# Performance work log

Measured on AMD Instinct MI355X. Metric: run time of the kernel, lower is better.

The kernel has to match this reference:

```python
import jax, jax.numpy as jnp
import numpy as np

DIM = 1024
NUM_HEADS = 16
HEAD_DIM = 64

def setup_inputs() -> dict:
    key = jax.random.key(0)
    ks = jax.random.split(key, 7)
    x = jax.random.normal(ks[0], (4, 4096, DIM), dtype=jnp.float32)
    mask = jnp.ones((4, 4096), dtype=jnp.float32)
    # torch Linear stores weight (out, in) and computes x @ W.T; we store (in, out) directly.
    Wq = jax.random.normal(ks[1], (DIM, NUM_HEADS * HEAD_DIM), dtype=jnp.float32) / np.sqrt(DIM)
    Wk = jax.random.normal(ks[2], (DIM, NUM_HEADS * HEAD_DIM), dtype=jnp.float32) / np.sqrt(DIM)
    Wv = jax.random.normal(ks[3], (DIM, NUM_HEADS * HEAD_DIM), dtype=jnp.float32) / np.sqrt(DIM)
    Wo = jax.random.normal(ks[4], (NUM_HEADS * HEAD_DIM, DIM), dtype=jnp.float32) / np.sqrt(NUM_HEADS * HEAD_DIM)
    # FeatureMap buffer: randn(dim, dim) / sqrt(dim) with dim = head_dim
    proj = jax.random.normal(ks[5], (HEAD_DIM, HEAD_DIM), dtype=jnp.float32) / np.sqrt(HEAD_DIM)
    return {"x": x, "mask": mask, "Wq": Wq, "Wk": Wk, "Wv": Wv, "Wo": Wo, "proj": proj}

def _feature_map(x, proj):
    # phi(x) = elu(x @ proj) + 1  (non-negative random features)
    return jax.nn.elu(x @ proj) + 1.0

def reference(x, mask, Wq, Wk, Wv, Wo, proj):
    b, n, _ = x.shape
    h, d = NUM_HEADS, HEAD_DIM
    # project and split heads: (b, h, n, d)
    q = (x @ Wq).reshape(b, n, h, d).transpose(0, 2, 1, 3)
    k = (x @ Wk).reshape(b, n, h, d).transpose(0, 2, 1, 3)
    v = (x @ Wv).reshape(b, n, h, d).transpose(0, 2, 1, 3)
    q = _feature_map(q, proj)
    k = _feature_map(k, proj)
    # mask: (b, n) -> (b, 1, n, 1)
    k = k * mask[:, None, :, None]
    # linear attention: phi(Q) (phi(K)^T V)
    kv = jnp.einsum('bhnd,bhne->bhde', k, v)          # (b, h, d, d)
    qkv = jnp.einsum('bhnd,bhde->bhne', q, kv)        # (b, h, n, d)
    k_sum = k.sum(axis=2)                              # (b, h, d)
    normalizer = jnp.einsum('bhnd,bhd->bhn', q, k_sum) + 1e-06
    out = qkv / normalizer[..., None]
    out = out.transpose(0, 2, 1, 3).reshape(b, n, h * d)
    return out @ Wo
```

## Files before the change

### kernel.cpp

```cpp
#include <hip/hip_runtime.h>
#include <stdint.h>

#define TOKENS 16384
#define KDIM 1024
#define QKVN 3072

typedef unsigned short u16;
using bf16x8 = __attribute__((ext_vector_type(8))) __bf16;
using f32x4  = __attribute__((ext_vector_type(4))) float;
using u16x8  = __attribute__((ext_vector_type(8))) unsigned short;

__device__ inline u16 f2bf(float f) {
  union { float f; uint32_t u; } v; v.f = f;
  uint32_t u = v.u;
  return (u16)((u + 0x7FFFu + ((u >> 16) & 1u)) >> 16);
}
__device__ inline float bf2f(u16 s) {
  union { uint32_t u; float f; } v; v.u = ((uint32_t)s) << 16;
  return v.f;
}
__device__ inline void g2l16(const void* g, void* l) {
  __builtin_amdgcn_global_load_lds(
      (const __attribute__((address_space(1))) void*)g,
      (__attribute__((address_space(3))) void*)l, 16, 0, 0);
}

template<int LD>
__device__ inline void stage_half(const u16* __restrict__ g, u16* l, int t) {
  #pragma unroll
  for (int i = 0; i < 2; ++i) {
    const int ch = i * 512 + t;
    const int row = ch >> 3;
    const int cc = (ch & 7) ^ (row & 7);
    g2l16(g + (long)row * LD + cc * 8, (char*)l + ch * 16);
  }
}

#define LDA_H(DST, BASE) do { \
  _Pragma("unroll") \
  for (int mi = 0; mi < 4; ++mi) { \
    const int row = wm*64 + mi*16 + rl; \
    const char* p = (const char*)(BASE) + row*128; \
    const int sw = (row & 7) << 4; \
    DST[mi][0] = *(const bf16x8*)(p + ((kg*16) ^ sw)); \
    DST[mi][1] = *(const bf16x8*)(p + ((64 + kg*16) ^ sw)); \
  } \
} while (0)

#define LDB_H(DST, BASE) do { \
  _Pragma("unroll") \
  for (int ni = 0; ni < 2; ++ni) { \
    const int row = wn*32 + ni*16 + rl; \
    const char* p = (const char*)(BASE) + row*128; \
    const int sw = (row & 7) << 4; \
    DST[ni][0] = *(const bf16x8*)(p + ((kg*16) ^ sw)); \
    DST[ni][1] = *(const bf16x8*)(p + ((64 + kg*16) ^ sw)); \
  } \
} while (0)

#define MFMAQ(MH, NH, AV, BV) do { \
  __builtin_amdgcn_s_setprio(1); \
  _Pragma("unroll") \
  for (int kh = 0; kh < 2; ++kh) \
    _Pragma("unroll") \
    for (int mi = 0; mi < 4; ++mi) \
      _Pragma("unroll") \
      for (int ni = 0; ni < 2; ++ni) \
        acc[(MH)*4+mi][(NH)*2+ni] = __builtin_amdgcn_mfma_f32_16x16x32_bf16( \
            AV[mi][kh], BV[ni][kh], acc[(MH)*4+mi][(NH)*2+ni], 0, 0, 0); \
  __builtin_amdgcn_s_setprio(0); \
} while (0)

#define LGKM0 do { \
  asm volatile("s_waitcnt lgkmcnt(0)" ::: "memory"); \
  __builtin_amdgcn_sched_barrier(0); \
} while (0)
#define LGKM_PRE(N) asm volatile("s_waitcnt lgkmcnt(" #N ")" ::: "memory")
#define VMC(N) asm volatile("s_waitcnt vmcnt(" #N ")" ::: "memory")
#define BAR() __builtin_amdgcn_s_barrier()

template<int NTOT, int EPI, int ALD, int NT, int PERB>
__global__ __launch_bounds__(512, 2) void gemm256(
    const u16* __restrict__ A, const u16* __restrict__ Bm,
    void* __restrict__ C, const float* __restrict__ aux) {
  __shared__ u16 As[2][2][8192];
  __shared__ u16 Bs[2][2][8192];
  const int t = threadIdx.x;
  const int l = t & 63;
  const int w = t >> 6;
  const int rl = l & 15, kg = l >> 4;
  const int wm = w >> 2, wn = w & 3;
  constexpr int nbn = NTOT / 256;
  constexpr int nwg = 64 * nbn;
  constexpr int GRID = nwg / NT;
  constexpr int KC = NT * 16;
  constexpr int IT = KC / 2;
  static_assert(nwg % 8 == 0, "bijective xcd swizzle");
  const int bid = blockIdx.x;

  auto tcoord = [&](int ot, long& tar, long& tbr) {
    const int gt = ot * GRID + bid;
    const int swz = (gt & 7) * (nwg / 8) + (gt >> 3);
    tar = (long)(swz / nbn) * 256;
    tbr = (long)(swz % nbn) * 256;
  };
  auto asrc = [&](int ch) {
    long ta, tb; tcoord(ch >> 4, ta, tb);
    return A + ta * ALD + (ch & 15) * 64;
  };
  auto bsrc = [&](int ch) {
    long ta, tb; tcoord(ch >> 4, ta, tb);
    return Bm + (PERB ? (ta >> 12) * 1048576 : 0) + tb * 1024 + (ch & 15) * 64;
  };

  f32x4 acc[8][4];
  #pragma unroll
  for (int i = 0; i < 8; ++i)
    #pragma unroll
    for (int j = 0; j < 4; ++j)
      acc[i][j] = (f32x4){0.f, 0.f, 0.f, 0.f};

  bf16x8 af[4][2], b0[2][2], b1[2][2];

  auto epilogue = [&](int ot) {
    long ar0, br0; tcoord(ot, ar0, br0);
    #pragma unroll
    for (int mh = 0; mh < 2; ++mh)
      #pragma unroll
      for (int mi = 0; mi < 4; ++mi)
        #pragma unroll
        for (int j = 0; j < 4; ++j) {
          const long row = ar0 + mh*128 + wm*64 + mi*16 + kg*4 + j;
          float rs = 0.f;
          if (EPI == 0) rs = aux[row];
          #pragma unroll
          for (int nh = 0; nh < 2; ++nh)
            #pragma unroll
            for (int ni = 0; ni < 2; ++ni) {
              const long col = br0 + nh*128 + wn*32 + ni*16 + rl;
              float v = acc[mh*4+mi][nh*2+ni][j];
              if (EPI == 0) {
                if (col < 2048) {
                  v = (v > 0.f) ? (v + 1.f) : __expf(v);
                  if (col >= 1024) v *= rs;
                }
                ((u16*)C)[row * QKVN + col] = f2bf(v);
              } else {
                ((float*)C)[row * NTOT + col] = v;
              }
            }
        }
    #pragma unroll
    for (int i = 0; i < 8; ++i)
      #pragma unroll
      for (int j = 0; j < 4; ++j)
        acc[i][j] = (f32x4){0.f, 0.f, 0.f, 0.f};
  };

  {
    const u16* A0s = asrc(0); const u16* B0s = bsrc(0);
    const u16* A1s = asrc(1); const u16* B1s = bsrc(1);
    stage_half<ALD >(A0s,             As[0][0], t);
    stage_half<1024>(B0s,             Bs[0][0], t);
    stage_half<1024>(B0s + 128*1024,  Bs[0][1], t);
    stage_half<ALD >(A0s + 128*ALD,   As[0][1], t);
    stage_half<ALD >(A1s,             As[1][0], t);
    stage_half<1024>(B1s,             Bs[1][0], t);
    stage_half<1024>(B1s + 128*1024,  Bs[1][1], t);
    VMC(6);
    BAR();
  }

  for (int i = 0; i < IT; ++i) {
    const int e = (2*i + 2 < KC) ? 2*i + 2 : KC - 1;
    const int o = (2*i + 3 < KC) ? 2*i + 3 : KC - 1;
    const u16* Ao1 = asrc(2*i + 1);
    const u16* Ae = asrc(e); const u16* Be = bsrc(e);
    const u16* Ao = asrc(o); const u16* Bo = bsrc(o);

    LDA_H(af, As[0][0]); LDB_H(b0, Bs[0][0]);
    stage_half<ALD>(Ao1 + 128*ALD, As[1][1], t);
    LGKM_PRE(8);
    BAR(); LGKM0;
    MFMAQ(0, 0, af, b0);
    BAR();
    LDB_H(b1, Bs[0][1]);
    stage_half<ALD>(Ae, As[0][0], t);
    BAR(); LGKM0;
    MFMAQ(0, 1, af, b1);
    BAR();
    LDA_H(af, As[0][1]);
    stage_half<1024>(Be, Bs[0][0], t);
    BAR(); LGKM0;
    MFMAQ(1, 0, af, b0);
    BAR();
    stage_half<1024>(Be + 128*1024, Bs[0][1], t);
    BAR();
    MFMAQ(1, 1, af, b1);
    VMC(6);
    BAR();
    LDA_H(af, As[1][0]); LDB_H(b0, Bs[1][0]);
    stage_half<ALD>(Ae + 128*ALD, As[0][1], t);
    LGKM_PRE(8);
    BAR(); LGKM0;
    MFMAQ(0, 0, af, b0);
    BAR();
    LDB_H(b1, Bs[1][1]);
    stage_half<ALD>(Ao, As[1][0], t);
    BAR(); LGKM0;
    MFMAQ(0, 1, af, b1);
    BAR();
    LDA_H(af, As[1][1]);
    stage_half<1024>(Bo, Bs[1][0], t);
    BAR(); LGKM0;
    MFMAQ(1, 0, af, b0);
    BAR();
    stage_half<1024>(Bo + 128*1024, Bs[1][1], t);
    BAR();
    MFMAQ(1, 1, af, b1);
    VMC(6);
    BAR();

    if ((i & 7) == 7) epilogue(i >> 3);
  }
  VMC(0);
}

__global__ __launch_bounds__(256) void kv_kernel(const u16* __restrict__ QKV,
    float* __restrict__ kvws, float* __restrict__ ksws) {
  __shared__ u16 Kl[32 * 64];
  __shared__ u16 Vl[32 * 64];
  const int t = threadIdx.x;
  const int l = t & 63, w = t >> 6;
  const int rl = l & 15, kg = l >> 4;
  const int bid = blockIdx.x;
  const int bh = bid >> 3, ns = bid & 7;
  const int b = bh >> 4, h = bh & 15;
  const long tok0 = (long)b * 4096 + ns * 512;

  f32x4 acc[4];
  #pragma unroll
  for (int i = 0; i < 4; ++i) acc[i] = (f32x4){0.f, 0.f, 0.f, 0.f};
  float ks = 0.f;
  const int srow = t >> 3, scc = t & 7;

  for (int it = 0; it < 16; ++it) {
    const long tb = tok0 + it * 32;
    g2l16(QKV + (tb + srow) * QKVN + 1024 + h * 64 + scc * 8, (char*)Kl + t * 16);
    g2l16(QKV + (tb + srow) * QKVN + 2048 + h * 64 + scc * 8, (char*)Vl + t * 16);
    __syncthreads();
    union { u16x8 u; bf16x8 v; } au, bu;
    #pragma unroll
    for (int j = 0; j < 8; ++j) au.u[j] = Kl[(kg * 8 + j) * 64 + w * 16 + rl];
    #pragma unroll
    for (int ni = 0; ni < 4; ++ni) {
      #pragma unroll
      for (int j = 0; j < 8; ++j) bu.u[j] = Vl[(kg * 8 + j) * 64 + ni * 16 + rl];
      acc[ni] = __builtin_amdgcn_mfma_f32_16x16x32_bf16(au.v, bu.v, acc[ni], 0, 0, 0);
    }
    #pragma unroll
    for (int r = 0; r < 8; ++r) ks += bf2f(Kl[(w * 8 + r) * 64 + (t & 63)]);
    __syncthreads();
  }
  float* kvb = kvws + bh * 4096;
  #pragma unroll
  for (int ni = 0; ni < 4; ++ni)
    #pragma unroll
    for (int j = 0; j < 4; ++j) {
      const int d = w * 16 + kg * 4 + j;
      const int e = ni * 16 + rl;
      atomicAdd(&kvb[d * 64 + e], acc[ni][j]);
    }
  atomicAdd(&ksws[bh * 64 + (t & 63)], ks);
}

__global__ __launch_bounds__(256) void scale_q(u16* __restrict__ QKV,
    const float* __restrict__ ksws) {
  __shared__ float ksl[1024];
  const int bid = blockIdx.x, t = threadIdx.x;
  const int n0 = bid * 16;
  const int b = n0 >> 12;
  #pragma unroll
  for (int i = 0; i < 4; ++i) ksl[i * 256 + t] = ksws[b * 1024 + i * 256 + t];
  __syncthreads();
  const int h = t & 15, ti = t >> 4;
  u16* qp = QKV + (long)(n0 + ti) * QKVN + h * 64;
  u16x8 v[8];
  float norm = 1e-6f;
  #pragma unroll
  for (int i = 0; i < 8; ++i) {
    v[i] = *(const u16x8*)(qp + i * 8);
    #pragma unroll
    for (int j = 0; j < 8; ++j) norm += bf2f(v[i][j]) * ksl[h * 64 + i * 8 + j];
  }
  const float inv = 1.0f / norm;
  #pragma unroll
  for (int i = 0; i < 8; ++i) {
    u16x8 o;
    #pragma unroll
    for (int j = 0; j < 8; ++j) o[j] = f2bf(bf2f(v[i][j]) * inv);
    *(u16x8*)(qp + i * 8) = o;
  }
}

__global__ __launch_bounds__(256) void w2_kernel(const float* __restrict__ kvws,
    const u16* __restrict__ WoT, u16* __restrict__ W2T) {
  __shared__ float kvl[64][64];
  const int bid = blockIdx.x, t = threadIdx.x;
  const int bh = bid >> 2, os = bid & 3;
  const int b = bh >> 4, h = bh & 15;
  const float* kvb = kvws + bh * 4096;
  #pragma unroll
  for (int i = 0; i < 16; ++i) ((float*)kvl)[i * 256 + t] = kvb[i * 256 + t];
  __syncthreads();
  const int o = os * 256 + t;
  float wo[64];
  const u16* wr = WoT + (long)o * 1024 + h * 64;
  #pragma unroll
  for (int i = 0; i < 8; ++i) {
    u16x8 v = *(const u16x8*)(wr + i * 8);
    #pragma unroll
    for (int j = 0; j < 8; ++j) wo[i * 8 + j] = bf2f(v[j]);
  }
  u16* out = W2T + (long)b * 1048576 + (long)o * 1024 + h * 64;
  for (int d = 0; d < 64; ++d) {
    float s = 0.f;
    #pragma unroll
    for (int e = 0; e < 64; ++e) s += wo[e] * kvl[d][e];
    out[d] = f2bf(s);
  }
}

__global__ __launch_bounds__(256) void prep_qk(const float* __restrict__ Wq,
    const float* __restrict__ Wk, const float* __restrict__ proj,
    u16* __restrict__ WqkvT) {
  __shared__ float Wl[128][65];
  __shared__ float Pl[64][65];
  const int bid = blockIdx.x;
  const int m = bid >> 7, h = (bid >> 3) & 15, cb = bid & 7;
  const float* W = m ? Wk : Wq;
  const int t = threadIdx.x;
  #pragma unroll
  for (int i = 0; i < 16; ++i) {
    const int idx = i * 256 + t;
    Pl[idx >> 6][idx & 63] = proj[idx];
  }
  #pragma unroll
  for (int i = 0; i < 32; ++i) {
    const int idx = i * 256 + t;
    const int c = idx >> 6, d = idx & 63;
    Wl[c][d] = W[(long)(cb * 128 + c) * 1024 + h * 64 + d];
  }
  __syncthreads();
  const int c = t & 127, j0 = (t >> 7) * 32;
  float a[32];
  #pragma unroll
  for (int jj = 0; jj < 32; ++jj) a[jj] = 0.f;
  for (int d = 0; d < 64; ++d) {
    const float wv = Wl[c][d];
    #pragma unroll
    for (int jj = 0; jj < 32; ++jj) a[jj] += wv * Pl[d][j0 + jj];
  }
  #pragma unroll
  for (int jj = 0; jj < 32; ++jj)
    WqkvT[(long)(m * 1024 + h * 64 + j0 + jj) * 1024 + cb * 128 + c] = f2bf(a[jj]);
}

__global__ __launch_bounds__(256) void prep_vo(const float* __restrict__ Wv,
    const float* __restrict__ Wo, u16* __restrict__ WqkvT, u16* __restrict__ WoT) {
  __shared__ float til[64][65];
  const int bid = blockIdx.x;
  const int which = bid >> 8, rt = (bid >> 4) & 15, ct = bid & 15;
  const float* S = which ? Wo : Wv;
  const int t = threadIdx.x;
  const int j = t & 63;
  #pragma unroll
  for (int p = 0; p < 16; ++p) {
    const int i = p * 4 + (t >> 6);
    til[i][j] = S[(long)(rt * 64 + i) * 1024 + ct * 64 + j];
  }
  __syncthreads();
  u16* dst = which ? WoT : (WqkvT + (long)2048 * 1024);
  #pragma unroll
  for (int p = 0; p < 16; ++p) {
    const int i = p * 4 + (t >> 6);
    dst[(long)(ct * 64 + i) * 1024 + rt * 64 + j] = f2bf(til[j][i]);
  }
}

__global__ __launch_bounds__(256) void conv_x(const float* __restrict__ x,
                                              u16* __restrict__ xb) {
  const int idx = blockIdx.x * 256 + threadIdx.x;
  const float4* p = (const float4*)x + (long)idx * 2;
  const float4 a = p[0], b = p[1];
  u16x8 o;
  o[0] = f2bf(a.x); o[1] = f2bf(a.y); o[2] = f2bf(a.z); o[3] = f2bf(a.w);
  o[4] = f2bf(b.x); o[5] = f2bf(b.y); o[6] = f2bf(b.z); o[7] = f2bf(b.w);
  *((u16x8*)xb + idx) = o;
}

extern "C" void kernel_launch(void* const* d_in, const int* in_sizes, int n_in,
                              void* d_out, int out_size, void* d_ws, size_t ws_size,
                              hipStream_t stream) {
  const float* x    = (const float*)d_in[0];
  const float* mask = (const float*)d_in[1];
  const float* Wq   = (const float*)d_in[2];
  const float* Wk   = (const float*)d_in[3];
  const float* Wv   = (const float*)d_in[4];
  const float* Wo   = (const float*)d_in[5];
  const float* proj = (const float*)d_in[6];

  char* ws = (char*)d_ws;
  u16*  WqkvT = (u16*)(ws);
  u16*  WoT   = (u16*)(ws + 6291456);
  u16*  xb    = (u16*)(ws + 8388608);
  u16*  QKV   = (u16*)(ws + 41943040);
  float* kvws = (float*)(ws + 142606336);
  float* ksws = (float*)(ws + 143654912);
  u16*  W2T  = (u16*)(ws + 8388608);
  if (ws_size < (size_t)143671296) return;

  hipMemsetAsync(kvws, 0, 1064960, stream);
  prep_qk<<<256, 256, 0, stream>>>(Wq, Wk, proj, WqkvT);
  prep_vo<<<512, 256, 0, stream>>>(Wv, Wo, WqkvT, WoT);
  conv_x <<<8192, 256, 0, stream>>>(x, xb);
  gemm256<3072, 0, 1024, 3, 0><<<256, 512, 0, stream>>>(xb, WqkvT, (void*)QKV, mask);
  kv_kernel<<<512, 256, 0, stream>>>(QKV, kvws, ksws);
  scale_q<<<1024, 256, 0, stream>>>((u16*)QKV, ksws);
  w2_kernel<<<256, 256, 0, stream>>>(kvws, WoT, W2T);
  gemm256<1024, 1, 3072, 1, 1><<<256, 512, 0, stream>>>(QKV, W2T, d_out, nullptr);
}
```

Measured before the change: 277.1 us.

## Restructure GEMM pipeline to four phases; compact Q and drop WoT prep

The GEMM main loop now loads both B halves at once and issues MFMAs across the full N width per phase. This halves the number of barrier-separated phases per k-chunk, at the cost of more live B fragment registers. scale_q writes the normalized Q into a compact 1024-wide buffer so the output GEMM reads A with stride 1024 instead of 3072. The separate Wo transpose/convert pass is removed, and w2_kernel reads fp32 Wo directly with strided loads.

```diff
diff --git a/kernel.cpp b/kernel.cpp
--- a/kernel.cpp
+++ b/kernel.cpp
@@ -58,16 +58,19 @@
   } \
 } while (0)
 
-#define MFMAQ(MH, NH, AV, BV) do { \
+#define MFMA2Q(MH, AV, BV0, BV1) do { \
   __builtin_amdgcn_s_setprio(1); \
   _Pragma("unroll") \
   for (int kh = 0; kh < 2; ++kh) \
     _Pragma("unroll") \
     for (int mi = 0; mi < 4; ++mi) \
       _Pragma("unroll") \
-      for (int ni = 0; ni < 2; ++ni) \
-        acc[(MH)*4+mi][(NH)*2+ni] = __builtin_amdgcn_mfma_f32_16x16x32_bf16( \
-            AV[mi][kh], BV[ni][kh], acc[(MH)*4+mi][(NH)*2+ni], 0, 0, 0); \
+      for (int ni = 0; ni < 2; ++ni) { \
+        acc[(MH)*4+mi][ni]   = __builtin_amdgcn_mfma_f32_16x16x32_bf16( \
+            AV[mi][kh], BV0[ni][kh], acc[(MH)*4+mi][ni], 0, 0, 0); \
+        acc[(MH)*4+mi][2+ni] = __builtin_amdgcn_mfma_f32_16x16x32_bf16( \
+            AV[mi][kh], BV1[ni][kh], acc[(MH)*4+mi][2+ni], 0, 0, 0); \
+      } \
   __builtin_amdgcn_s_setprio(0); \
 } while (0)
 
@@ -120,7 +123,7 @@
     for (int j = 0; j < 4; ++j)
       acc[i][j] = (f32x4){0.f, 0.f, 0.f, 0.f};
 
-  bf16x8 af[4][2], b0[2][2], b1[2][2];
+  bf16x8 afA[4][2], bA[2][2], bB[2][2];
 
   auto epilogue = [&](int ot) {
     long ar0, br0; tcoord(ot, ar0, br0);
@@ -166,60 +169,47 @@
     stage_half<ALD >(A0s + 128*ALD,   As[0][1], t);
     stage_half<ALD >(A1s,             As[1][0], t);
     stage_half<1024>(B1s,             Bs[1][0], t);
-    stage_half<1024>(B1s + 128*1024,  Bs[1][1], t);
-    VMC(6);
+    VMC(4);
     BAR();
   }
 
   for (int i = 0; i < IT; ++i) {
+    const int o1 = 2*i + 1;
     const int e = (2*i + 2 < KC) ? 2*i + 2 : KC - 1;
     const int o = (2*i + 3 < KC) ? 2*i + 3 : KC - 1;
-    const u16* Ao1 = asrc(2*i + 1);
-    const u16* Ae = asrc(e); const u16* Be = bsrc(e);
-    const u16* Ao = asrc(o); const u16* Bo = bsrc(o);
-
-    LDA_H(af, As[0][0]); LDB_H(b0, Bs[0][0]);
+    const u16* Ao1 = asrc(o1); const u16* Bo1 = bsrc(o1);
+    const u16* Ae = asrc(e);   const u16* Be = bsrc(e);
+    const u16* Ao = asrc(o);   const u16* Bo = bsrc(o);
+
+    LDA_H(afA, As[0][0]); LDB_H(bA, Bs[0][0]); LDB_H(bB, Bs[0][1]);
     stage_half<ALD>(Ao1 + 128*ALD, As[1][1], t);
+    stage_half<1024>(Bo1 + 128*1024, Bs[1][1], t);
     LGKM_PRE(8);
     BAR(); LGKM0;
-    MFMAQ(0, 0, af, b0);
-    BAR();
-    LDB_H(b1, Bs[0][1]);
+    MFMA2Q(0, afA, bA, bB);
+    VMC(4); BAR();
+
+    LDA_H(afA, As[0][1]);
     stage_half<ALD>(Ae, As[0][0], t);
-    BAR(); LGKM0;
-    MFMAQ(0, 1, af, b1);
-    BAR();
-    LDA_H(af, As[0][1]);
     stage_half<1024>(Be, Bs[0][0], t);
     BAR(); LGKM0;
-    MFMAQ(1, 0, af, b0);
-    BAR();
+    MFMA2Q(1, afA, bA, bB);
+    VMC(4); BAR();
+
+    LDA_H(afA, As[1][0]); LDB_H(bA, Bs[1][0]); LDB_H(bB, Bs[1][1]);
+    stage_half<ALD>(Ae + 128*ALD, As[0][1], t);
     stage_half<1024>(Be + 128*1024, Bs[0][1], t);
-    BAR();
-    MFMAQ(1, 1, af, b1);
-    VMC(6);
-    BAR();
-    LDA_H(af, As[1][0]); LDB_H(b0, Bs[1][0]);
-    stage_half<ALD>(Ae + 128*ALD, As[0][1], t);
     LGKM_PRE(8);
     BAR(); LGKM0;
-    MFMAQ(0, 0, af, b0);
-    BAR();
-    LDB_H(b1, Bs[1][1]);
+    MFMA2Q(0, afA, bA, bB);
+    VMC(4); BAR();
+
+    LDA_H(afA, As[1][1]);
     stage_half<ALD>(Ao, As[1][0], t);
-    BAR(); LGKM0;
-    MFMAQ(0, 1, af, b1);
-    BAR();
-    LDA_H(af, As[1][1]);
     stage_half<1024>(Bo, Bs[1][0], t);
     BAR(); LGKM0;
-    MFMAQ(1, 0, af, b0);
-    BAR();
-    stage_half<1024>(Bo + 128*1024, Bs[1][1], t);
-    BAR();
-    MFMAQ(1, 1, af, b1);
-    VMC(6);
-    BAR();
+    MFMA2Q(1, afA, bA, bB);
+    VMC(4); BAR();
 
     if ((i & 7) == 7) epilogue(i >> 3);
   }
@@ -274,8 +264,8 @@
   atomicAdd(&ksws[bh * 64 + (t & 63)], ks);
 }
 
-__global__ __launch_bounds__(256) void scale_q(u16* __restrict__ QKV,
-    const float* __restrict__ ksws) {
+__global__ __launch_bounds__(256) void scale_q(const u16* __restrict__ QKV,
+    const float* __restrict__ ksws, u16* __restrict__ Qc) {
   __shared__ float ksl[1024];
   const int bid = blockIdx.x, t = threadIdx.x;
   const int n0 = bid * 16;
@@ -284,7 +274,8 @@
   for (int i = 0; i < 4; ++i) ksl[i * 256 + t] = ksws[b * 1024 + i * 256 + t];
   __syncthreads();
   const int h = t & 15, ti = t >> 4;
-  u16* qp = QKV + (long)(n0 + ti) * QKVN + h * 64;
+  const u16* qp = QKV + (long)(n0 + ti) * QKVN + h * 64;
+  u16* op = Qc + (long)(n0 + ti) * 1024 + h * 64;
   u16x8 v[8];
   float norm = 1e-6f;
   #pragma unroll
@@ -299,12 +290,12 @@
     u16x8 o;
     #pragma unroll
     for (int j = 0; j < 8; ++j) o[j] = f2bf(bf2f(v[i][j]) * inv);
-    *(u16x8*)(qp + i * 8) = o;
+    *(u16x8*)(op + i * 8) = o;
   }
 }
 
 __global__ __launch_bounds__(256) void w2_kernel(const float* __restrict__ kvws,
-    const u16* __restrict__ WoT, u16* __restrict__ W2T) {
+    const float* __restrict__ Wo, u16* __restrict__ W2T) {
   __shared__ float kvl[64][64];
   const int bid = blockIdx.x, t = threadIdx.x;
   const int bh = bid >> 2, os = bid & 3;
@@ -315,13 +306,8 @@
   __syncthreads();
   const int o = os * 256 + t;
   float wo[64];
-  const u16* wr = WoT + (long)o * 1024 + h * 64;
-  #pragma unroll
-  for (int i = 0; i < 8; ++i) {
-    u16x8 v = *(const u16x8*)(wr + i * 8);
-    #pragma unroll
-    for (int j = 0; j < 8; ++j) wo[i * 8 + j] = bf2f(v[j]);
-  }
+  #pragma unroll
+  for (int e = 0; e < 64; ++e) wo[e] = Wo[(long)(h * 64 + e) * 1024 + o];
   u16* out = W2T + (long)b * 1048576 + (long)o * 1024 + h * 64;
   for (int d = 0; d < 64; ++d) {
     float s = 0.f;
@@ -366,21 +352,20 @@
     WqkvT[(long)(m * 1024 + h * 64 + j0 + jj) * 1024 + cb * 128 + c] = f2bf(a[jj]);
 }
 
-__global__ __launch_bounds__(256) void prep_vo(const float* __restrict__ Wv,
-    const float* __restrict__ Wo, u16* __restrict__ WqkvT, u16* __restrict__ WoT) {
+__global__ __launch_bounds__(256) void prep_v(const float* __restrict__ Wv,
+    u16* __restrict__ WqkvT) {
   __shared__ float til[64][65];
   const int bid = blockIdx.x;
-  const int which = bid >> 8, rt = (bid >> 4) & 15, ct = bid & 15;
-  const float* S = which ? Wo : Wv;
+  const int rt = (bid >> 4) & 15, ct = bid & 15;
   const int t = threadIdx.x;
   const int j = t & 63;
   #pragma unroll
   for (int p = 0; p < 16; ++p) {
     const int i = p * 4 + (t >> 6);
-    til[i][j] = S[(long)(rt * 64 + i) * 1024 + ct * 64 + j];
+    til[i][j] = Wv[(long)(rt * 64 + i) * 1024 + ct * 64 + j];
   }
   __syncthreads();
-  u16* dst = which ? WoT : (WqkvT + (long)2048 * 1024);
+  u16* dst = WqkvT + (long)2048 * 1024;
   #pragma unroll
   for (int p = 0; p < 16; ++p) {
     const int i = p * 4 + (t >> 6);
@@ -412,21 +397,21 @@
 
   char* ws = (char*)d_ws;
   u16*  WqkvT = (u16*)(ws);
-  u16*  WoT   = (u16*)(ws + 6291456);
   u16*  xb    = (u16*)(ws + 8388608);
   u16*  QKV   = (u16*)(ws + 41943040);
   float* kvws = (float*)(ws + 142606336);
   float* ksws = (float*)(ws + 143654912);
-  u16*  W2T  = (u16*)(ws + 8388608);
+  u16*  Qc   = xb;
+  u16*  W2T  = (u16*)(ws);
   if (ws_size < (size_t)143671296) return;
 
   hipMemsetAsync(kvws, 0, 1064960, stream);
   prep_qk<<<256, 256, 0, stream>>>(Wq, Wk, proj, WqkvT);
-  prep_vo<<<512, 256, 0, stream>>>(Wv, Wo, WqkvT, WoT);
+  prep_v <<<256, 256, 0, stream>>>(Wv, WqkvT);
   conv_x <<<8192, 256, 0, stream>>>(x, xb);
   gemm256<3072, 0, 1024, 3, 0><<<256, 512, 0, stream>>>(xb, WqkvT, (void*)QKV, mask);
   kv_kernel<<<512, 256, 0, stream>>>(QKV, kvws, ksws);
-  scale_q<<<1024, 256, 0, stream>>>((u16*)QKV, ksws);
-  w2_kernel<<<256, 256, 0, stream>>>(kvws, WoT, W2T);
-  gemm256<1024, 1, 3072, 1, 1><<<256, 512, 0, stream>>>(QKV, W2T, d_out, nullptr);
-}
+  scale_q<<<1024, 256, 0, stream>>>(QKV, ksws, Qc);
+  w2_kernel<<<256, 256, 0, stream>>>(kvws, Wo, W2T);
+  gemm256<1024, 1, 1024, 1, 1><<<256, 512, 0, stream>>>(Qc, W2T, d_out, nullptr);
+}
```

Result: faster. 269.7 us (-2.7%).
